# Kernel optimization log

Hardware: AMD Instinct MI355X
Metric: run time of the kernel (lower is better)

The kernel has to match this reference:

```python
import jax, jax.numpy as jnp
import numpy as np

N_GRAPHS = 1024
N_NODES = 65536
N_EDGES = 262144
D = 256          # node/edge/global feature dim
D_IN = 3 * D     # concat of edge_agg, node_agg, globals
D_HID = 512
D_OUT = 256


def setup_inputs() -> dict:
    key = jax.random.key(0)
    ks = jax.random.split(key, 9)
    nodes = jax.random.normal(ks[0], (N_NODES, D), dtype=jnp.float32)
    edges = jax.random.normal(ks[1], (N_EDGES, D), dtype=jnp.float32)
    globals_ = jax.random.normal(ks[2], (N_GRAPHS, D), dtype=jnp.float32)
    node_graph_ids = jnp.sort(jax.random.randint(ks[3], (N_NODES,), 0, N_GRAPHS, dtype=jnp.int32))
    edge_graph_ids = jnp.sort(jax.random.randint(ks[4], (N_EDGES,), 0, N_GRAPHS, dtype=jnp.int32))
    W1 = jax.random.normal(ks[5], (D_IN, D_HID), dtype=jnp.float32) * (1.0 / np.sqrt(D_IN))
    b1 = jnp.zeros((D_HID,), dtype=jnp.float32)
    W2 = jax.random.normal(ks[6], (D_HID, D_OUT), dtype=jnp.float32) * (1.0 / np.sqrt(D_HID))
    b2 = jnp.zeros((D_OUT,), dtype=jnp.float32)
    return {"nodes": nodes, "edges": edges, "globals_": globals_,
            "node_graph_ids": node_graph_ids, "edge_graph_ids": edge_graph_ids,
            "W1": W1, "b1": b1, "W2": W2, "b2": b2}


def reference(nodes, edges, globals_, node_graph_ids, edge_graph_ids, W1, b1, W2, b2):
    G = globals_.shape[0]
    # EdgesToGlobalsAggregator / NodesToGlobalsAggregator: unsorted segment sum per graph
    edge_agg = jax.ops.segment_sum(edges, edge_graph_ids, num_segments=G)  # [G, D]
    node_agg = jax.ops.segment_sum(nodes, node_graph_ids, num_segments=G)  # [G, D]
    collected = jnp.concatenate([edge_agg, node_agg, globals_], axis=-1)   # [G, 3D]
    # global_model: 2-layer MLP with ReLU
    h = jax.nn.relu(collected @ W1 + b1)
    updated_globals = h @ W2 + b2
    return updated_globals
```

## Files before the change

kernel.cpp:

```cpp
#include <hip/hip_runtime.h>

#define G      1024
#define NNODES 65536
#define NEDGES 262144
#define D      256
#define DIN    768
#define DHID   512
#define DOUT   256
#define CW     512

#define AGG_BLOCKS 1024
#define EROWS      64
#define NROWS      16

__device__ __forceinline__ void flush_acc(float* __restrict__ dst, int cur, int col,
                                          float4& acc) {
    float* p = dst + (size_t)cur * CW + col;
    atomicAdd(p + 0, acc.x); atomicAdd(p + 1, acc.y);
    atomicAdd(p + 2, acc.z); atomicAdd(p + 3, acc.w);
    acc.x = acc.y = acc.z = acc.w = 0.f;
}

__device__ __forceinline__ void row_step(int id, const float4 v, int& cur, float4& acc,
                                         float* __restrict__ dst, int col) {
    if (id != cur) { flush_acc(dst, cur, col, acc); cur = id; }
    acc.x += v.x; acc.y += v.y; acc.z += v.z; acc.w += v.w;
}

__device__ __forceinline__ void load_group(const float4* __restrict__ src,
                                           const int* __restrict__ ids, int r, int lane,
                                           float4 v[8], int4& i0, int4& i1) {
    const float4* p = src + (size_t)r * (D / 4) + lane;
#pragma unroll
    for (int j = 0; j < 8; ++j) v[j] = p[j * (D / 4)];
    i0 = *(const int4*)&ids[r];
    i1 = *(const int4*)&ids[r + 4];
}

__device__ __forceinline__ void proc_group(const float4 v[8], int4 i0, int4 i1,
                                           int& cur, float4& acc,
                                           float* __restrict__ dst, int col) {
    if (i0.x == cur && i1.w == cur) {
        acc.x += ((v[0].x + v[1].x) + (v[2].x + v[3].x)) + ((v[4].x + v[5].x) + (v[6].x + v[7].x));
        acc.y += ((v[0].y + v[1].y) + (v[2].y + v[3].y)) + ((v[4].y + v[5].y) + (v[6].y + v[7].y));
        acc.z += ((v[0].z + v[1].z) + (v[2].z + v[3].z)) + ((v[4].z + v[5].z) + (v[6].z + v[7].z));
        acc.w += ((v[0].w + v[1].w) + (v[2].w + v[3].w)) + ((v[4].w + v[5].w) + (v[6].w + v[7].w));
    } else {
        row_step(i0.x, v[0], cur, acc, dst, col);
        row_step(i0.y, v[1], cur, acc, dst, col);
        row_step(i0.z, v[2], cur, acc, dst, col);
        row_step(i0.w, v[3], cur, acc, dst, col);
        row_step(i1.x, v[4], cur, acc, dst, col);
        row_step(i1.y, v[5], cur, acc, dst, col);
        row_step(i1.z, v[6], cur, acc, dst, col);
        row_step(i1.w, v[7], cur, acc, dst, col);
    }
}

__device__ __forceinline__ void seg_sum_pipelined(
        const float4* __restrict__ src, const int* __restrict__ ids,
        float* __restrict__ dst, int col, int r, int ngroups, int lane) {
    float4 va[8], vb[8];
    int4 ia0, ia1, ib0, ib1;
    float4 acc = {0.f, 0.f, 0.f, 0.f};
    int cur = ids[r];

    load_group(src, ids, r, lane, va, ia0, ia1);
    for (int gpair = 0; gpair < ngroups / 2 - 1; ++gpair) {
        load_group(src, ids, r + 8, lane, vb, ib0, ib1);
        proc_group(va, ia0, ia1, cur, acc, dst, col);
        r += 8;
        load_group(src, ids, r + 8, lane, va, ia0, ia1);
        proc_group(vb, ib0, ib1, cur, acc, dst, col);
        r += 8;
    }
    load_group(src, ids, r + 8, lane, vb, ib0, ib1);
    proc_group(va, ia0, ia1, cur, acc, dst, col);
    proc_group(vb, ib0, ib1, cur, acc, dst, col);
    flush_acc(dst, cur, col, acc);
}

__global__ __launch_bounds__(256, 4) void fused_agg(
        const float4* __restrict__ nodes,
        const float4* __restrict__ edges,
        const int* __restrict__ nids,
        const int* __restrict__ eids,
        float* __restrict__ collected) {
    const int lane = threadIdx.x & 63;
    const int wave = threadIdx.x >> 6;
    const int W    = blockIdx.x * 4 + wave;

    seg_sum_pipelined(edges, eids, collected, lane * 4,       W * EROWS, EROWS / 8, lane);
    seg_sum_pipelined(nodes, nids, collected, D + lane * 4,   W * NROWS, NROWS / 8, lane);
}

__global__ __launch_bounds__(256) void gemm_bias_act(
        const float* __restrict__ A1, const float* __restrict__ A2,
        const float* __restrict__ B,
        const float* __restrict__ bias, float* __restrict__ C,
        int N, int K, int asplit, int s1, int s2, int relu) {
    __shared__ float At[2][32][34];
    __shared__ __align__(16) float Bs[2][32][64];

    const int tid = threadIdx.x;
    const int tx = tid & 15;
    const int ty = tid >> 4;
    const int m0 = blockIdx.y * 32;
    const int n0 = blockIdx.x * 64;

    const int ar = tid >> 3;
    const int ac = (tid & 7) * 4;
    const int br = tid >> 3;
    const int bc = (tid & 7) * 8;

    const int arow = m0 + ar;
    const float* Bptr = B + (size_t)br * N + n0 + bc;

    auto loadA = [&](int kc) -> float4 {
        return (kc < asplit) ? *(const float4*)&A1[(size_t)arow * s1 + kc + ac]
                             : *(const float4*)&A2[(size_t)arow * s2 + (kc - asplit) + ac];
    };

    {
        const float4 a4  = loadA(0);
        const float4 b40 = *(const float4*)Bptr;
        const float4 b41 = *(const float4*)(Bptr + 4);
        At[0][ac + 0][ar] = a4.x; At[0][ac + 1][ar] = a4.y;
        At[0][ac + 2][ar] = a4.z; At[0][ac + 3][ar] = a4.w;
        *(float4*)&Bs[0][br][bc]     = b40;
        *(float4*)&Bs[0][br][bc + 4] = b41;
    }
    __syncthreads();

    float4 acc0 = {0.f, 0.f, 0.f, 0.f};
    float4 acc1 = {0.f, 0.f, 0.f, 0.f};
    int buf = 0;

    for (int kt = 0; kt < K; kt += 32) {
        const bool has_next = (kt + 32) < K;
        float4 na, nb0, nb1;
        if (has_next) {
            na  = loadA(kt + 32);
            nb0 = *(const float4*)(Bptr + (size_t)(kt + 32) * N);
            nb1 = *(const float4*)(Bptr + (size_t)(kt + 32) * N + 4);
        }
#pragma unroll
        for (int k = 0; k < 32; ++k) {
            const float2 a2 = *(const float2*)&At[buf][k][ty * 2];
            const float4 bv = *(const float4*)&Bs[buf][k][tx * 4];
            acc0.x += a2.x * bv.x; acc0.y += a2.x * bv.y;
            acc0.z += a2.x * bv.z; acc0.w += a2.x * bv.w;
            acc1.x += a2.y * bv.x; acc1.y += a2.y * bv.y;
            acc1.z += a2.y * bv.z; acc1.w += a2.y * bv.w;
        }
        if (has_next) {
            const int nb = buf ^ 1;
            At[nb][ac + 0][ar] = na.x; At[nb][ac + 1][ar] = na.y;
            At[nb][ac + 2][ar] = na.z; At[nb][ac + 3][ar] = na.w;
            *(float4*)&Bs[nb][br][bc]     = nb0;
            *(float4*)&Bs[nb][br][bc + 4] = nb1;
            __syncthreads();
            buf = nb;
        }
    }

    const int col = n0 + tx * 4;
    const int row = m0 + ty * 2;
    const float4 bv = *(const float4*)&bias[col];
    float4 o0, o1;
    o0.x = acc0.x + bv.x; o0.y = acc0.y + bv.y; o0.z = acc0.z + bv.z; o0.w = acc0.w + bv.w;
    o1.x = acc1.x + bv.x; o1.y = acc1.y + bv.y; o1.z = acc1.z + bv.z; o1.w = acc1.w + bv.w;
    if (relu) {
        o0.x = fmaxf(o0.x, 0.f); o0.y = fmaxf(o0.y, 0.f);
        o0.z = fmaxf(o0.z, 0.f); o0.w = fmaxf(o0.w, 0.f);
        o1.x = fmaxf(o1.x, 0.f); o1.y = fmaxf(o1.y, 0.f);
        o1.z = fmaxf(o1.z, 0.f); o1.w = fmaxf(o1.w, 0.f);
    }
    *(float4*)&C[(size_t)row * N + col] = o0;
    *(float4*)&C[(size_t)(row + 1) * N + col] = o1;
}

extern "C" void kernel_launch(void* const* d_in, const int* in_sizes, int n_in,
                              void* d_out, int out_size, void* d_ws, size_t ws_size,
                              hipStream_t stream) {
    const float* nodes    = (const float*)d_in[0];
    const float* edges    = (const float*)d_in[1];
    const float* globals_ = (const float*)d_in[2];
    const int*   nids     = (const int*)d_in[3];
    const int*   eids     = (const int*)d_in[4];
    const float* W1       = (const float*)d_in[5];
    const float* b1       = (const float*)d_in[6];
    const float* W2       = (const float*)d_in[7];
    const float* b2       = (const float*)d_in[8];
    float* out = (float*)d_out;

    float* collected = (float*)d_ws;
    float* h         = collected + (size_t)G * CW;

    hipMemsetAsync(collected, 0, (size_t)G * CW * sizeof(float), stream);

    fused_agg<<<AGG_BLOCKS, 256, 0, stream>>>(
        (const float4*)nodes, (const float4*)edges, nids, eids, collected);

    gemm_bias_act<<<dim3(DHID / 64, G / 32), 256, 0, stream>>>(
        collected, globals_, W1, b1, h, DHID, DIN, CW, CW, D, 1);

    gemm_bias_act<<<dim3(DOUT / 64, G / 32), 256, 0, stream>>>(
        h, h, W2, b2, out, DOUT, DHID, DHID, DHID, DHID, 0);
}
```

Baseline: 456.1 us.

## Fuse both MLP layers into one kernel with split-K atomic output

Merges the two GEMM launches into one kernel. Each block computes a 32x64 tile of the hidden layer, keeps it in shared memory, and multiplies it by the matching 64 rows of W2. The partial outputs are accumulated into a zeroed output with atomics, and bias b2 is added only by the first hidden-chunk block. This removes the h round trip through global memory and one launch, in exchange for an extra memset, 8-way atomic contention on each output element, and non-deterministic summation order.

```diff
diff --git a/kernel.cpp b/kernel.cpp
--- a/kernel.cpp
+++ b/kernel.cpp
@@ -94,19 +94,21 @@
     seg_sum_pipelined(nodes, nids, collected, D + lane * 4,   W * NROWS, NROWS / 8, lane);
 }
 
-__global__ __launch_bounds__(256) void gemm_bias_act(
+__global__ __launch_bounds__(256) void mlp_fused(
         const float* __restrict__ A1, const float* __restrict__ A2,
-        const float* __restrict__ B,
-        const float* __restrict__ bias, float* __restrict__ C,
-        int N, int K, int asplit, int s1, int s2, int relu) {
+        const float* __restrict__ W1, const float* __restrict__ b1,
+        const float* __restrict__ W2, const float* __restrict__ b2,
+        float* __restrict__ out) {
     __shared__ float At[2][32][34];
     __shared__ __align__(16) float Bs[2][32][64];
+    __shared__ __align__(16) float Hs[32][64];
 
     const int tid = threadIdx.x;
     const int tx = tid & 15;
     const int ty = tid >> 4;
+    const int hc = blockIdx.x;
     const int m0 = blockIdx.y * 32;
-    const int n0 = blockIdx.x * 64;
+    const int n0 = hc * 64;
 
     const int ar = tid >> 3;
     const int ac = (tid & 7) * 4;
@@ -114,11 +116,11 @@
     const int bc = (tid & 7) * 8;
 
     const int arow = m0 + ar;
-    const float* Bptr = B + (size_t)br * N + n0 + bc;
+    const float* Bptr = W1 + (size_t)br * DHID + n0 + bc;
 
     auto loadA = [&](int kc) -> float4 {
-        return (kc < asplit) ? *(const float4*)&A1[(size_t)arow * s1 + kc + ac]
-                             : *(const float4*)&A2[(size_t)arow * s2 + (kc - asplit) + ac];
+        return (kc < CW) ? *(const float4*)&A1[(size_t)arow * CW + kc + ac]
+                         : *(const float4*)&A2[(size_t)arow * D + (kc - CW) + ac];
     };
 
     {
@@ -136,13 +138,13 @@
     float4 acc1 = {0.f, 0.f, 0.f, 0.f};
     int buf = 0;
 
-    for (int kt = 0; kt < K; kt += 32) {
-        const bool has_next = (kt + 32) < K;
+    for (int kt = 0; kt < DIN; kt += 32) {
+        const bool has_next = (kt + 32) < DIN;
         float4 na, nb0, nb1;
         if (has_next) {
             na  = loadA(kt + 32);
-            nb0 = *(const float4*)(Bptr + (size_t)(kt + 32) * N);
-            nb1 = *(const float4*)(Bptr + (size_t)(kt + 32) * N + 4);
+            nb0 = *(const float4*)(Bptr + (size_t)(kt + 32) * DHID);
+            nb1 = *(const float4*)(Bptr + (size_t)(kt + 32) * DHID + 4);
         }
 #pragma unroll
         for (int k = 0; k < 32; ++k) {
@@ -164,20 +166,51 @@
         }
     }
 
-    const int col = n0 + tx * 4;
-    const int row = m0 + ty * 2;
-    const float4 bv = *(const float4*)&bias[col];
-    float4 o0, o1;
-    o0.x = acc0.x + bv.x; o0.y = acc0.y + bv.y; o0.z = acc0.z + bv.z; o0.w = acc0.w + bv.w;
-    o1.x = acc1.x + bv.x; o1.y = acc1.y + bv.y; o1.z = acc1.z + bv.z; o1.w = acc1.w + bv.w;
-    if (relu) {
-        o0.x = fmaxf(o0.x, 0.f); o0.y = fmaxf(o0.y, 0.f);
-        o0.z = fmaxf(o0.z, 0.f); o0.w = fmaxf(o0.w, 0.f);
-        o1.x = fmaxf(o1.x, 0.f); o1.y = fmaxf(o1.y, 0.f);
-        o1.z = fmaxf(o1.z, 0.f); o1.w = fmaxf(o1.w, 0.f);
-    }
-    *(float4*)&C[(size_t)row * N + col] = o0;
-    *(float4*)&C[(size_t)(row + 1) * N + col] = o1;
+    {
+        const float4 bv = *(const float4*)&b1[n0 + tx * 4];
+        float4 o0, o1;
+        o0.x = fmaxf(acc0.x + bv.x, 0.f); o0.y = fmaxf(acc0.y + bv.y, 0.f);
+        o0.z = fmaxf(acc0.z + bv.z, 0.f); o0.w = fmaxf(acc0.w + bv.w, 0.f);
+        o1.x = fmaxf(acc1.x + bv.x, 0.f); o1.y = fmaxf(acc1.y + bv.y, 0.f);
+        o1.z = fmaxf(acc1.z + bv.z, 0.f); o1.w = fmaxf(acc1.w + bv.w, 0.f);
+        *(float4*)&Hs[ty * 2][tx * 4]     = o0;
+        *(float4*)&Hs[ty * 2 + 1][tx * 4] = o1;
+    }
+    __syncthreads();
+
+    const int c2 = (tid & 63) * 4;
+    const int rg = tid >> 6;
+    float acc2[8][4] = {};
+    const float* W2p = W2 + (size_t)n0 * DOUT + c2;
+#pragma unroll 4
+    for (int k0 = 0; k0 < 64; k0 += 4) {
+        float4 w[4];
+#pragma unroll
+        for (int j = 0; j < 4; ++j)
+            w[j] = *(const float4*)(W2p + (size_t)(k0 + j) * DOUT);
+#pragma unroll
+        for (int r = 0; r < 8; ++r) {
+            const float4 h4 = *(const float4*)&Hs[rg * 8 + r][k0];
+            acc2[r][0] += h4.x * w[0].x + h4.y * w[1].x + h4.z * w[2].x + h4.w * w[3].x;
+            acc2[r][1] += h4.x * w[0].y + h4.y * w[1].y + h4.z * w[2].y + h4.w * w[3].y;
+            acc2[r][2] += h4.x * w[0].z + h4.y * w[1].z + h4.z * w[2].z + h4.w * w[3].z;
+            acc2[r][3] += h4.x * w[0].w + h4.y * w[1].w + h4.z * w[2].w + h4.w * w[3].w;
+        }
+    }
+    if (hc == 0) {
+        const float4 b = *(const float4*)&b2[c2];
+#pragma unroll
+        for (int r = 0; r < 8; ++r) {
+            acc2[r][0] += b.x; acc2[r][1] += b.y;
+            acc2[r][2] += b.z; acc2[r][3] += b.w;
+        }
+    }
+#pragma unroll
+    for (int r = 0; r < 8; ++r) {
+        float* p = out + (size_t)(m0 + rg * 8 + r) * DOUT + c2;
+        atomicAdd(p + 0, acc2[r][0]); atomicAdd(p + 1, acc2[r][1]);
+        atomicAdd(p + 2, acc2[r][2]); atomicAdd(p + 3, acc2[r][3]);
+    }
 }
 
 extern "C" void kernel_launch(void* const* d_in, const int* in_sizes, int n_in,
@@ -195,16 +228,13 @@
     float* out = (float*)d_out;
 
     float* collected = (float*)d_ws;
-    float* h         = collected + (size_t)G * CW;
 
     hipMemsetAsync(collected, 0, (size_t)G * CW * sizeof(float), stream);
+    hipMemsetAsync(out, 0, (size_t)G * DOUT * sizeof(float), stream);
 
     fused_agg<<<AGG_BLOCKS, 256, 0, stream>>>(
         (const float4*)nodes, (const float4*)edges, nids, eids, collected);
 
-    gemm_bias_act<<<dim3(DHID / 64, G / 32), 256, 0, stream>>>(
-        collected, globals_, W1, b1, h, DHID, DIN, CW, CW, D, 1);
-
-    gemm_bias_act<<<dim3(DOUT / 64, G / 32), 256, 0, stream>>>(
-        h, h, W2, b2, out, DOUT, DHID, DHID, DHID, DHID, 0);
-}
+    mlp_fused<<<dim3(DHID / 64, G / 32), 256, 0, stream>>>(
+        collected, globals_, W1, b1, W2, b2, out);
+}
```

Result: slower. 496.1 us (+8.8%).

## Aggregate per graph via binary search, drop atomics and memset; smaller GEMM2 tiles

Applied to the files above, without the earlier changes.

The atomic-based segment sum over fixed row chunks is replaced by one block per graph. Each block finds its segment bounds by binary search on the sorted ids, reduces the rows across 4 waves, combines them in shared memory and writes the result directly. This removes the memset and all the atomics, at the cost of load imbalance from uneven segment sizes and less memory-level parallelism per wave. The second GEMM also gets a 16-row tile so it launches more blocks and fills more CUs.

```diff
diff --git a/kernel.cpp b/kernel.cpp
--- a/kernel.cpp
+++ b/kernel.cpp
@@ -9,89 +9,72 @@
 #define DOUT   256
 #define CW     512
 
-#define AGG_BLOCKS 1024
-#define EROWS      64
-#define NROWS      16
-
-__device__ __forceinline__ void flush_acc(float* __restrict__ dst, int cur, int col,
-                                          float4& acc) {
-    float* p = dst + (size_t)cur * CW + col;
-    atomicAdd(p + 0, acc.x); atomicAdd(p + 1, acc.y);
-    atomicAdd(p + 2, acc.z); atomicAdd(p + 3, acc.w);
-    acc.x = acc.y = acc.z = acc.w = 0.f;
-}
-
-__device__ __forceinline__ void row_step(int id, const float4 v, int& cur, float4& acc,
-                                         float* __restrict__ dst, int col) {
-    if (id != cur) { flush_acc(dst, cur, col, acc); cur = id; }
-    acc.x += v.x; acc.y += v.y; acc.z += v.z; acc.w += v.w;
-}
-
-__device__ __forceinline__ void load_group(const float4* __restrict__ src,
-                                           const int* __restrict__ ids, int r, int lane,
-                                           float4 v[8], int4& i0, int4& i1) {
-    const float4* p = src + (size_t)r * (D / 4) + lane;
-#pragma unroll
-    for (int j = 0; j < 8; ++j) v[j] = p[j * (D / 4)];
-    i0 = *(const int4*)&ids[r];
-    i1 = *(const int4*)&ids[r + 4];
-}
-
-__device__ __forceinline__ void proc_group(const float4 v[8], int4 i0, int4 i1,
-                                           int& cur, float4& acc,
-                                           float* __restrict__ dst, int col) {
-    if (i0.x == cur && i1.w == cur) {
-        acc.x += ((v[0].x + v[1].x) + (v[2].x + v[3].x)) + ((v[4].x + v[5].x) + (v[6].x + v[7].x));
-        acc.y += ((v[0].y + v[1].y) + (v[2].y + v[3].y)) + ((v[4].y + v[5].y) + (v[6].y + v[7].y));
-        acc.z += ((v[0].z + v[1].z) + (v[2].z + v[3].z)) + ((v[4].z + v[5].z) + (v[6].z + v[7].z));
-        acc.w += ((v[0].w + v[1].w) + (v[2].w + v[3].w)) + ((v[4].w + v[5].w) + (v[6].w + v[7].w));
-    } else {
-        row_step(i0.x, v[0], cur, acc, dst, col);
-        row_step(i0.y, v[1], cur, acc, dst, col);
-        row_step(i0.z, v[2], cur, acc, dst, col);
-        row_step(i0.w, v[3], cur, acc, dst, col);
-        row_step(i1.x, v[4], cur, acc, dst, col);
-        row_step(i1.y, v[5], cur, acc, dst, col);
-        row_step(i1.z, v[6], cur, acc, dst, col);
-        row_step(i1.w, v[7], cur, acc, dst, col);
-    }
-}
-
-__device__ __forceinline__ void seg_sum_pipelined(
-        const float4* __restrict__ src, const int* __restrict__ ids,
-        float* __restrict__ dst, int col, int r, int ngroups, int lane) {
-    float4 va[8], vb[8];
-    int4 ia0, ia1, ib0, ib1;
+
+__device__ __forceinline__ int lb_sorted(const int* __restrict__ a, int n, int v) {
+    int lo = 0, hi = n;
+    while (lo < hi) { int m = (lo + hi) >> 1; if (a[m] < v) lo = m + 1; else hi = m; }
+    return lo;
+}
+
+__device__ __forceinline__ float4 seg_sum_rows(const float4* __restrict__ src,
+                                               int s, int e, int w, int lane) {
     float4 acc = {0.f, 0.f, 0.f, 0.f};
-    int cur = ids[r];
-
-    load_group(src, ids, r, lane, va, ia0, ia1);
-    for (int gpair = 0; gpair < ngroups / 2 - 1; ++gpair) {
-        load_group(src, ids, r + 8, lane, vb, ib0, ib1);
-        proc_group(va, ia0, ia1, cur, acc, dst, col);
-        r += 8;
-        load_group(src, ids, r + 8, lane, va, ia0, ia1);
-        proc_group(vb, ib0, ib1, cur, acc, dst, col);
-        r += 8;
-    }
-    load_group(src, ids, r + 8, lane, vb, ib0, ib1);
-    proc_group(va, ia0, ia1, cur, acc, dst, col);
-    proc_group(vb, ib0, ib1, cur, acc, dst, col);
-    flush_acc(dst, cur, col, acc);
-}
-
-__global__ __launch_bounds__(256, 4) void fused_agg(
+    const int n = e - s;
+    const int ngrp = n >> 2;
+    for (int gi = w; gi < ngrp; gi += 4) {
+        const float4* p = src + (size_t)(s + gi * 4) * (D / 4) + lane;
+        const float4 v0 = p[0];
+        const float4 v1 = p[D / 4];
+        const float4 v2 = p[2 * (D / 4)];
+        const float4 v3 = p[3 * (D / 4)];
+        acc.x += (v0.x + v1.x) + (v2.x + v3.x);
+        acc.y += (v0.y + v1.y) + (v2.y + v3.y);
+        acc.z += (v0.z + v1.z) + (v2.z + v3.z);
+        acc.w += (v0.w + v1.w) + (v2.w + v3.w);
+    }
+    if (w == 0) {
+        for (int r = s + (ngrp << 2); r < e; ++r) {
+            const float4 v = src[(size_t)r * (D / 4) + lane];
+            acc.x += v.x; acc.y += v.y; acc.z += v.z; acc.w += v.w;
+        }
+    }
+    return acc;
+}
+
+__global__ __launch_bounds__(256, 4) void agg_per_graph(
         const float4* __restrict__ nodes,
         const float4* __restrict__ edges,
         const int* __restrict__ nids,
         const int* __restrict__ eids,
         float* __restrict__ collected) {
-    const int lane = threadIdx.x & 63;
-    const int wave = threadIdx.x >> 6;
-    const int W    = blockIdx.x * 4 + wave;
-
-    seg_sum_pipelined(edges, eids, collected, lane * 4,       W * EROWS, EROWS / 8, lane);
-    seg_sum_pipelined(nodes, nids, collected, D + lane * 4,   W * NROWS, NROWS / 8, lane);
+    __shared__ int seg[4];
+    __shared__ float ered[4][256];
+    __shared__ float nred[4][256];
+
+    const int tid  = threadIdx.x;
+    const int lane = tid & 63;
+    const int w    = tid >> 6;
+    const int g    = blockIdx.x;
+
+    if (tid < 4) {
+        const int* a = (tid < 2) ? eids : nids;
+        const int  n = (tid < 2) ? NEDGES : NNODES;
+        seg[tid] = lb_sorted(a, n, g + (tid & 1));
+    }
+    __syncthreads();
+    const int es = seg[0], ee = seg[1], ns = seg[2], ne = seg[3];
+
+    const float4 ea = seg_sum_rows(edges, es, ee, w, lane);
+    const float4 na = seg_sum_rows(nodes, ns, ne, w, lane);
+
+    *(float4*)&ered[w][lane * 4] = ea;
+    *(float4*)&nred[w][lane * 4] = na;
+    __syncthreads();
+
+    const float ev = (ered[0][tid] + ered[1][tid]) + (ered[2][tid] + ered[3][tid]);
+    const float nv = (nred[0][tid] + nred[1][tid]) + (nred[2][tid] + nred[3][tid]);
+    collected[(size_t)g * CW + tid]       = ev;
+    collected[(size_t)g * CW + 256 + tid] = nv;
 }
 
 __global__ __launch_bounds__(256) void gemm_bias_act(
@@ -178,6 +161,78 @@
     }
     *(float4*)&C[(size_t)row * N + col] = o0;
     *(float4*)&C[(size_t)(row + 1) * N + col] = o1;
+}
+
+__global__ __launch_bounds__(256) void gemm2_bias(
+        const float* __restrict__ A, const float* __restrict__ B,
+        const float* __restrict__ bias, float* __restrict__ C) {
+    __shared__ float At[2][32][17];
+    __shared__ __align__(16) float Bs[2][32][64];
+
+    const int tid = threadIdx.x;
+    const int tx = tid & 15;
+    const int ty = tid >> 4;
+    const int m0 = blockIdx.y * 16;
+    const int n0 = blockIdx.x * 64;
+
+    const int ar = (tid >> 3) & 15;
+    const int ac = (tid & 7) * 4;
+    const int br = tid >> 3;
+    const int bc = (tid & 7) * 8;
+
+    const float* Aptr = A + (size_t)(m0 + ar) * DHID + ac;
+    const float* Bptr = B + (size_t)br * DOUT + n0 + bc;
+
+    {
+        const float4 b40 = *(const float4*)Bptr;
+        const float4 b41 = *(const float4*)(Bptr + 4);
+        *(float4*)&Bs[0][br][bc]     = b40;
+        *(float4*)&Bs[0][br][bc + 4] = b41;
+        if (tid < 128) {
+            const float4 a4 = *(const float4*)Aptr;
+            At[0][ac + 0][ar] = a4.x; At[0][ac + 1][ar] = a4.y;
+            At[0][ac + 2][ar] = a4.z; At[0][ac + 3][ar] = a4.w;
+        }
+    }
+    __syncthreads();
+
+    float4 acc = {0.f, 0.f, 0.f, 0.f};
+    int buf = 0;
+
+    for (int kt = 0; kt < DHID; kt += 32) {
+        const bool has_next = (kt + 32) < DHID;
+        float4 na, nb0, nb1;
+        if (has_next) {
+            nb0 = *(const float4*)(Bptr + (size_t)(kt + 32) * DOUT);
+            nb1 = *(const float4*)(Bptr + (size_t)(kt + 32) * DOUT + 4);
+            if (tid < 128) na = *(const float4*)(Aptr + (kt + 32));
+        }
+#pragma unroll
+        for (int k = 0; k < 32; ++k) {
+            const float a   = At[buf][k][ty];
+            const float4 bv = *(const float4*)&Bs[buf][k][tx * 4];
+            acc.x += a * bv.x; acc.y += a * bv.y;
+            acc.z += a * bv.z; acc.w += a * bv.w;
+        }
+        if (has_next) {
+            const int nb = buf ^ 1;
+            *(float4*)&Bs[nb][br][bc]     = nb0;
+            *(float4*)&Bs[nb][br][bc + 4] = nb1;
+            if (tid < 128) {
+                At[nb][ac + 0][ar] = na.x; At[nb][ac + 1][ar] = na.y;
+                At[nb][ac + 2][ar] = na.z; At[nb][ac + 3][ar] = na.w;
+            }
+            __syncthreads();
+            buf = nb;
+        }
+    }
+
+    const int col = n0 + tx * 4;
+    const float4 bv = *(const float4*)&bias[col];
+    float4 o;
+    o.x = acc.x + bv.x; o.y = acc.y + bv.y;
+    o.z = acc.z + bv.z; o.w = acc.w + bv.w;
+    *(float4*)&C[(size_t)(m0 + ty) * DOUT + col] = o;
 }
 
 extern "C" void kernel_launch(void* const* d_in, const int* in_sizes, int n_in,
@@ -197,14 +252,12 @@
     float* collected = (float*)d_ws;
     float* h         = collected + (size_t)G * CW;
 
-    hipMemsetAsync(collected, 0, (size_t)G * CW * sizeof(float), stream);
-
-    fused_agg<<<AGG_BLOCKS, 256, 0, stream>>>(
+
+    agg_per_graph<<<G, 256, 0, stream>>>(
         (const float4*)nodes, (const float4*)edges, nids, eids, collected);
 
     gemm_bias_act<<<dim3(DHID / 64, G / 32), 256, 0, stream>>>(
         collected, globals_, W1, b1, h, DHID, DIN, CW, CW, D, 1);
 
-    gemm_bias_act<<<dim3(DOUT / 64, G / 32), 256, 0, stream>>>(
-        h, h, W2, b2, out, DOUT, DHID, DHID, DHID, DHID, 0);
-}
+    gemm2_bias<<<dim3(DOUT / 64, G / 16), 256, 0, stream>>>(h, W2, b2, out);
+}
```

New measurement: 455.3 us. Within noise of the previous version (-0.2%).
